# Performance work log

Hardware: AMD Instinct MI355X
Metric: run time of the kernel (lower is better)

## Reference

```python
import jax, jax.numpy as jnp
import numpy as np


def _cell(x, h, c, Wih, Whh, bih, bhh):
    # PyTorch LSTM cell, gate order i, f, g, o
    g = x @ Wih.T + h @ Whh.T + bih + bhh
    i, f, gg, o = jnp.split(g, 4, axis=-1)
    c = jax.nn.sigmoid(f) * c + jax.nn.sigmoid(i) * jnp.tanh(gg)
    h = jax.nn.sigmoid(o) * jnp.tanh(c)
    return h, c


def _run_layer(x, Wih, Whh, bih, bhh):
    # x: (B, T, I) -> (hs (B,T,H), hT (B,H), cT (B,H))
    B = x.shape[0]
    H = Whh.shape[1]
    h0 = jnp.zeros((B, H), x.dtype)
    c0 = jnp.zeros((B, H), x.dtype)

    def step(carry, xt):
        h, c = carry
        h, c = _cell(xt, h, c, Wih, Whh, bih, bhh)
        return (h, c), h

    (hT, cT), hs = jax.lax.scan(step, (h0, c0), jnp.swapaxes(x, 0, 1))
    return jnp.swapaxes(hs, 0, 1), hT, cT


def setup_inputs() -> dict:
    key = jax.random.key(0)
    B, T_HIST, F, H, T_FUT = 16384, 20, 10, 128, 30
    s = 0.08  # ~1/sqrt(hidden) init scale
    ks = jax.random.split(key, 20)
    inp = {
        'hist':   jax.random.normal(ks[0], (B, T_HIST, F), jnp.float32),
        'e_Wih0': jax.random.normal(ks[1], (4 * H, F), jnp.float32) * s,
        'e_Whh0': jax.random.normal(ks[2], (4 * H, H), jnp.float32) * s,
        'e_bih0': jax.random.normal(ks[3], (4 * H,), jnp.float32) * s,
        'e_bhh0': jax.random.normal(ks[4], (4 * H,), jnp.float32) * s,
        'e_Wih1': jax.random.normal(ks[5], (4 * H, H), jnp.float32) * s,
        'e_Whh1': jax.random.normal(ks[6], (4 * H, H), jnp.float32) * s,
        'e_bih1': jax.random.normal(ks[7], (4 * H,), jnp.float32) * s,
        'e_bhh1': jax.random.normal(ks[8], (4 * H,), jnp.float32) * s,
        'd_Wih0': jax.random.normal(ks[9], (4 * H, 2), jnp.float32) * s,
        'd_Whh0': jax.random.normal(ks[10], (4 * H, H), jnp.float32) * s,
        'd_bih0': jax.random.normal(ks[11], (4 * H,), jnp.float32) * s,
        'd_bhh0': jax.random.normal(ks[12], (4 * H,), jnp.float32) * s,
        'd_Wih1': jax.random.normal(ks[13], (4 * H, H), jnp.float32) * s,
        'd_Whh1': jax.random.normal(ks[14], (4 * H, H), jnp.float32) * s,
        'd_bih1': jax.random.normal(ks[15], (4 * H,), jnp.float32) * s,
        'd_bhh1': jax.random.normal(ks[16], (4 * H,), jnp.float32) * s,
        'head_W': jax.random.normal(ks[17], (2, H), jnp.float32) * s,
        'head_b': jax.random.normal(ks[18], (2,), jnp.float32) * s,
        'fut_len': T_FUT,
    }
    return inp


def reference(hist, e_Wih0, e_Whh0, e_bih0, e_bhh0, e_Wih1, e_Whh1, e_bih1, e_bhh1,
              d_Wih0, d_Whh0, d_bih0, d_bhh0, d_Wih1, d_Whh1, d_bih1, d_bhh1,
              head_W, head_b, fut_len):
    B = hist.shape[0]
    # 2-layer encoder over history
    h1, hT0, cT0 = _run_layer(hist, e_Wih0, e_Whh0, e_bih0, e_bhh0)
    _, hT1, cT1 = _run_layer(h1, e_Wih1, e_Whh1, e_bih1, e_bhh1)

    def step(carry, _):
        y, h0, c0, h1_, c1_ = carry
        nh0, nc0 = _cell(y, h0, c0, d_Wih0, d_Whh0, d_bih0, d_bhh0)
        nh1, nc1 = _cell(nh0, h1_, c1_, d_Wih1, d_Whh1, d_bih1, d_bhh1)
        dxy = nh1 @ head_W.T + head_b  # (B, 2)
        return (dxy, nh0, nc0, nh1, nc1), dxy

    y0 = jnp.zeros((B, 2), hist.dtype)
    _, ys = jax.lax.scan(step, (y0, hT0, cT0, hT1, cT1), None, length=fut_len)
    return jnp.swapaxes(ys, 0, 1)  # (B, fut_len, 2)
```

## Files before the change

kernel.cpp:

```cpp
#include <hip/hip_runtime.h>


typedef __attribute__((ext_vector_type(8))) short short8;
typedef __attribute__((ext_vector_type(4))) float float4v;

#define MFMA16(a, b, c) __builtin_amdgcn_mfma_f32_16x16x32_bf16((a), (b), (c), 0, 0, 0)

__device__ __forceinline__ unsigned short f2bf(float x) {
    unsigned u = __builtin_bit_cast(unsigned, x);
    unsigned r = (u + 0x7FFFu + ((u >> 16) & 1u)) >> 16;
    return (unsigned short)r;
}
__device__ __forceinline__ float bf2f(unsigned short b) {
    unsigned u = ((unsigned)b) << 16;
    return __builtin_bit_cast(float, u);
}

#if __has_builtin(__builtin_amdgcn_exp2f)
__device__ __forceinline__ float vexp2(float x) { return __builtin_amdgcn_exp2f(x); }
#else
__device__ __forceinline__ float vexp2(float x) { return exp2f(x); }
#endif
#if __has_builtin(__builtin_amdgcn_rcpf)
__device__ __forceinline__ float vrcp(float x) { return __builtin_amdgcn_rcpf(x); }
#else
__device__ __forceinline__ float vrcp(float x) { return 1.0f / x; }
#endif

__device__ __forceinline__ float sigm(float x) {
    return vrcp(1.0f + vexp2(x * -1.442695040888963f));
}
__device__ __forceinline__ float tanh_(float x) {
    return 1.0f - 2.0f * vrcp(1.0f + vexp2(x * 2.885390081777927f));
}

__global__ void prep_kernel(const float* __restrict__ eWih0, const float* __restrict__ eWhh0,
                            const float* __restrict__ ebih0, const float* __restrict__ ebhh0,
                            const float* __restrict__ eWih1, const float* __restrict__ eWhh1,
                            const float* __restrict__ ebih1, const float* __restrict__ ebhh1,
                            const float* __restrict__ dWih0, const float* __restrict__ dWhh0,
                            const float* __restrict__ dbih0, const float* __restrict__ dbhh0,
                            const float* __restrict__ dWih1, const float* __restrict__ dWhh1,
                            const float* __restrict__ dbih1, const float* __restrict__ dbhh1,
                            void* __restrict__ ws)
{
    int i = blockIdx.x * 256 + threadIdx.x;
    short* We0 = (short*)ws;
    short* We1 = We0 + 512 * 160;
    short* Wd0 = We1 + 512 * 256;
    short* Wd1 = Wd0 + 512 * 128;
    float* bsT = (float*)((char*)ws + 819200);
    float* wyT = bsT + 2048;
    const int N0 = 512 * 160, N1 = 512 * 256, N2 = 512 * 128, N3 = 512 * 256;
    if (i < N0) {
        int n = i / 160, k = i - n * 160;
        float v = (k < 32) ? (k < 10 ? eWih0[n * 10 + k] : 0.0f) : eWhh0[n * 128 + (k - 32)];
        We0[i] = (short)f2bf(v);
    } else if (i < N0 + N1) {
        int ii = i - N0, n = ii >> 8, k = ii & 255;
        float v = (k < 128) ? eWih1[n * 128 + k] : eWhh1[n * 128 + (k - 128)];
        We1[ii] = (short)f2bf(v);
    } else if (i < N0 + N1 + N2) {
        int ii = i - (N0 + N1);
        Wd0[ii] = (short)f2bf(dWhh0[ii]);
    } else if (i < N0 + N1 + N2 + N3) {
        int ii = i - (N0 + N1 + N2), n = ii >> 8, k = ii & 255;
        float v = (k < 128) ? dWih1[n * 128 + k] : dWhh1[n * 128 + (k - 128)];
        Wd1[ii] = (short)f2bf(v);
    } else if (i < N0 + N1 + N2 + N3 + 2048) {
        int ii = i - (N0 + N1 + N2 + N3);
        int set = ii >> 9, r = ii & 511, j = r >> 2, q = r & 3;
        int g = q * 128 + j;
        float v = (set == 0) ? ebih0[g] + ebhh0[g]
                : (set == 1) ? ebih1[g] + ebhh1[g]
                : (set == 2) ? dbih0[g] + dbhh0[g]
                             : dbih1[g] + dbhh1[g];
        bsT[ii] = v;
    } else if (i < N0 + N1 + N2 + N3 + 2048 + 1024) {
        int ii = i - (N0 + N1 + N2 + N3 + 2048);
        int j = ii >> 3, e = ii & 7, q = e >> 1, cc = e & 1;
        wyT[ii] = dWih0[(q * 128 + j) * 2 + cc];
    }
}


template <int NKT>
__device__ __forceinline__ void mma4(float4v acc[4][4], const short8* __restrict__ hb,
                                     const char* __restrict__ wb, const unsigned* wo,
                                     int woff, int nib, int quad)
{
#pragma unroll 1
    for (int kk = 0; kk < NKT; ++kk) {
        int sx = ((kk * 4 + quad) ^ nib) + nib * 16;
        short8 a0 = hb[sx];
        short8 a1 = hb[256 + sx];
        short8 a2 = hb[512 + sx];
        short8 a3 = hb[768 + sx];
        short8 b0 = *(const short8*)(wb + (wo[0] + woff + kk * 64));
        short8 b1 = *(const short8*)(wb + (wo[1] + woff + kk * 64));
        short8 b2 = *(const short8*)(wb + (wo[2] + woff + kk * 64));
        short8 b3 = *(const short8*)(wb + (wo[3] + woff + kk * 64));
        acc[0][0] = MFMA16(a0, b0, acc[0][0]);
        acc[0][1] = MFMA16(a1, b0, acc[0][1]);
        acc[0][2] = MFMA16(a2, b0, acc[0][2]);
        acc[0][3] = MFMA16(a3, b0, acc[0][3]);
        acc[1][0] = MFMA16(a0, b1, acc[1][0]);
        acc[1][1] = MFMA16(a1, b1, acc[1][1]);
        acc[1][2] = MFMA16(a2, b1, acc[1][2]);
        acc[1][3] = MFMA16(a3, b1, acc[1][3]);
        acc[2][0] = MFMA16(a0, b2, acc[2][0]);
        acc[2][1] = MFMA16(a1, b2, acc[2][1]);
        acc[2][2] = MFMA16(a2, b2, acc[2][2]);
        acc[2][3] = MFMA16(a3, b2, acc[2][3]);
        acc[3][0] = MFMA16(a0, b3, acc[3][0]);
        acc[3][1] = MFMA16(a1, b3, acc[3][1]);
        acc[3][2] = MFMA16(a2, b3, acc[3][2]);
        acc[3][3] = MFMA16(a3, b3, acc[3][3]);
    }
}

template <bool DEC0>
__device__ __forceinline__ void cell_update4(float4v acc[4][4], float4v bv,
                                             float* __restrict__ cbase,
                                             unsigned short* __restrict__ hdst,
                                             const float* __restrict__ ybuf,
                                             float4v wy0, float4v wy1,
                                             int j, int quad)
{
    int kc = j >> 3;
    int jl = j & 7;
#pragma unroll
    for (int mt = 0; mt < 4; ++mt) {
#pragma unroll
        for (int r = 0; r < 4; ++r) {
            float gi = acc[0][mt][r] + bv[0];
            float gf = acc[1][mt][r] + bv[1];
            float gg = acc[2][mt][r] + bv[2];
            float go = acc[3][mt][r] + bv[3];
            int m = mt * 16 + quad * 4 + r;
            if (DEC0) {
                float y0 = ybuf[2 * m], y1 = ybuf[2 * m + 1];
                gi += y0 * wy0[0] + y1 * wy0[1];
                gf += y0 * wy0[2] + y1 * wy0[3];
                gg += y0 * wy1[0] + y1 * wy1[1];
                go += y0 * wy1[2] + y1 * wy1[3];
            }
            float si = sigm(gi);
            float sf = sigm(gf);
            float tg = tanh_(gg);
            float so = sigm(go);
            float* cp = cbase + (m * 132 + j);
            float c = sf * (*cp) + si * tg;
            *cp = c;
            float h = so * tanh_(c);
            int slot = m * 16 + (kc ^ (m & 15));
            hdst[slot * 8 + jl] = f2bf(h);
        }
    }
}

__global__ void __attribute__((amdgpu_flat_work_group_size(512, 512), amdgpu_waves_per_eu(2)))
lstm_main(
    const float* __restrict__ hist,
    const float* __restrict__ headW, const float* __restrict__ headB,
    const int* __restrict__ futlen, const void* __restrict__ ws,
    float* __restrict__ out)
{
    __shared__ short8 h0buf[1024];
    __shared__ short8 h1buf[1024];
    __shared__ short8 xbuf[256];
    __shared__ float ybuf[128];
    __shared__ float cbuf0[64 * 132];
    __shared__ float cbuf1[64 * 132];

    const char* wsb = (const char*)ws;
    const char* We0 = wsb;
    const char* We1 = wsb + 512 * 160 * 2;
    const char* Wd0 = We1 + 512 * 256 * 2;
    const char* Wd1 = Wd0 + 512 * 128 * 2;
    const float* bsT = (const float*)(wsb + 819200);
    const float* wyT = bsT + 2048;

    const int tid = threadIdx.x;
    const int w = tid >> 6;
    const int lane = tid & 63;
    const int quad = lane >> 4;
    const int nib = lane & 15;
    const int b0 = blockIdx.x * 64;
    const int TFUT = *futlen;
    const int j = 16 * w + nib;

    h0buf[tid] = (short8)0;
    h0buf[512 + tid] = (short8)0;
    h1buf[tid] = (short8)0;
    h1buf[512 + tid] = (short8)0;
    if (tid < 256) xbuf[tid] = (short8)0;
    if (tid < 128) ybuf[tid] = 0.0f;
    for (int i = tid; i < 64 * 132; i += 512) {
        cbuf0[i] = 0.0f;
        cbuf1[i] = 0.0f;
    }

    unsigned eo0[4], eo1[4];
#pragma unroll
    for (int q = 0; q < 4; ++q) {
        unsigned row = 16u * (w + 8 * q) + nib;
        eo0[q] = row * 320u + quad * 16u;
        eo1[q] = row * 512u + quad * 16u;
    }
    __syncthreads();

#pragma unroll 1
    for (int t = 0; t < 20; ++t) {
        if (tid < 128) {
            int m = tid & 63, part = tid >> 6;
            const float* hp = hist + ((size_t)((b0 + m) * 20 + t)) * 10;
            float v[8];
            if (part == 0) {
#pragma unroll
                for (int i = 0; i < 8; ++i) v[i] = hp[i];
            } else {
                v[0] = hp[8]; v[1] = hp[9];
#pragma unroll
                for (int i = 2; i < 8; ++i) v[i] = 0.0f;
            }
            short8 pk;
#pragma unroll
            for (int i = 0; i < 8; ++i) pk[i] = (short)f2bf(v[i]);
            xbuf[m * 4 + (part ^ (m & 3))] = pk;
        }
        __syncthreads();

        {
            float4v acc[4][4];
#pragma unroll
            for (int q = 0; q < 4; ++q)
#pragma unroll
                for (int mt = 0; mt < 4; ++mt) acc[q][mt] = (float4v){0.f, 0.f, 0.f, 0.f};
            {
                int sxx = (quad ^ (nib & 3)) + nib * 4;
                short8 a0 = xbuf[sxx];
                short8 a1 = xbuf[64 + sxx];
                short8 a2 = xbuf[128 + sxx];
                short8 a3 = xbuf[192 + sxx];
                short8 bq0 = *(const short8*)(We0 + eo0[0]);
                short8 bq1 = *(const short8*)(We0 + eo0[1]);
                short8 bq2 = *(const short8*)(We0 + eo0[2]);
                short8 bq3 = *(const short8*)(We0 + eo0[3]);
                acc[0][0] = MFMA16(a0, bq0, acc[0][0]);
                acc[0][1] = MFMA16(a1, bq0, acc[0][1]);
                acc[0][2] = MFMA16(a2, bq0, acc[0][2]);
                acc[0][3] = MFMA16(a3, bq0, acc[0][3]);
                acc[1][0] = MFMA16(a0, bq1, acc[1][0]);
                acc[1][1] = MFMA16(a1, bq1, acc[1][1]);
                acc[1][2] = MFMA16(a2, bq1, acc[1][2]);
                acc[1][3] = MFMA16(a3, bq1, acc[1][3]);
                acc[2][0] = MFMA16(a0, bq2, acc[2][0]);
                acc[2][1] = MFMA16(a1, bq2, acc[2][1]);
                acc[2][2] = MFMA16(a2, bq2, acc[2][2]);
                acc[2][3] = MFMA16(a3, bq2, acc[2][3]);
                acc[3][0] = MFMA16(a0, bq3, acc[3][0]);
                acc[3][1] = MFMA16(a1, bq3, acc[3][1]);
                acc[3][2] = MFMA16(a2, bq3, acc[3][2]);
                acc[3][3] = MFMA16(a3, bq3, acc[3][3]);
            }
            mma4<4>(acc, h0buf, We0, eo0, 64, nib, quad);
            float4v bv = *(const float4v*)(bsT + 0 * 512 + j * 4);
            __syncthreads();
            cell_update4<false>(acc, bv, cbuf0, (unsigned short*)h0buf, nullptr,
                                (float4v){0, 0, 0, 0}, (float4v){0, 0, 0, 0}, j, quad);
        }
        __syncthreads();

        {
            float4v acc[4][4];
#pragma unroll
            for (int q = 0; q < 4; ++q)
#pragma unroll
                for (int mt = 0; mt < 4; ++mt) acc[q][mt] = (float4v){0.f, 0.f, 0.f, 0.f};
            mma4<4>(acc, h0buf, We1, eo1, 0, nib, quad);
            mma4<4>(acc, h1buf, We1, eo1, 256, nib, quad);
            float4v bv = *(const float4v*)(bsT + 1 * 512 + j * 4);
            __syncthreads();
            cell_update4<false>(acc, bv, cbuf1, (unsigned short*)h1buf, nullptr,
                                (float4v){0, 0, 0, 0}, (float4v){0, 0, 0, 0}, j, quad);
        }
        __syncthreads();
    }

    unsigned do0[4];
#pragma unroll
    for (int q = 0; q < 4; ++q) {
        unsigned row = 16u * (w + 8 * q) + nib;
        do0[q] = row * 256u + quad * 16u;
    }

#pragma unroll 1
    for (int t = 0; t < TFUT; ++t) {
        {
            float4v acc[4][4];
#pragma unroll
            for (int q = 0; q < 4; ++q)
#pragma unroll
                for (int mt = 0; mt < 4; ++mt) acc[q][mt] = (float4v){0.f, 0.f, 0.f, 0.f};
            mma4<4>(acc, h0buf, Wd0, do0, 0, nib, quad);
            float4v bv = *(const float4v*)(bsT + 2 * 512 + j * 4);
            float4v wy0 = *(const float4v*)(wyT + j * 8);
            float4v wy1 = *(const float4v*)(wyT + j * 8 + 4);
            __syncthreads();
            cell_update4<true>(acc, bv, cbuf0, (unsigned short*)h0buf, ybuf, wy0, wy1, j, quad);
        }
        __syncthreads();

        {
            float4v acc[4][4];
#pragma unroll
            for (int q = 0; q < 4; ++q)
#pragma unroll
                for (int mt = 0; mt < 4; ++mt) acc[q][mt] = (float4v){0.f, 0.f, 0.f, 0.f};
            mma4<4>(acc, h0buf, Wd1, eo1, 0, nib, quad);
            mma4<4>(acc, h1buf, Wd1, eo1, 256, nib, quad);
            float4v bv = *(const float4v*)(bsT + 3 * 512 + j * 4);
            __syncthreads();
            cell_update4<false>(acc, bv, cbuf1, (unsigned short*)h1buf, nullptr,
                                (float4v){0, 0, 0, 0}, (float4v){0, 0, 0, 0}, j, quad);
        }
        __syncthreads();

        if (tid < 128) {
            int m = tid & 63, jj = tid >> 6;
            const float4v* hw = (const float4v*)(headW + jj * 128);
            float dot = headB[jj];
            int mk = m & 15;
#pragma unroll
            for (int kc = 0; kc < 16; ++kc) {
                short8 ch = h1buf[m * 16 + (kc ^ mk)];
                float4v w0 = hw[kc * 2], w1 = hw[kc * 2 + 1];
                dot += bf2f((unsigned short)ch[0]) * w0[0];
                dot += bf2f((unsigned short)ch[1]) * w0[1];
                dot += bf2f((unsigned short)ch[2]) * w0[2];
                dot += bf2f((unsigned short)ch[3]) * w0[3];
                dot += bf2f((unsigned short)ch[4]) * w1[0];
                dot += bf2f((unsigned short)ch[5]) * w1[1];
                dot += bf2f((unsigned short)ch[6]) * w1[2];
                dot += bf2f((unsigned short)ch[7]) * w1[3];
            }
            ybuf[2 * m + jj] = dot;
            out[((size_t)(b0 + m) * TFUT + t) * 2 + jj] = dot;
        }
        __syncthreads();
    }
}

extern "C" void kernel_launch(void* const* d_in, const int* in_sizes, int n_in,
                              void* d_out, int out_size, void* d_ws, size_t ws_size,
                              hipStream_t stream)
{
    const float* hist   = (const float*)d_in[0];
    const float* eWih0  = (const float*)d_in[1];
    const float* eWhh0  = (const float*)d_in[2];
    const float* ebih0  = (const float*)d_in[3];
    const float* ebhh0  = (const float*)d_in[4];
    const float* eWih1  = (const float*)d_in[5];
    const float* eWhh1  = (const float*)d_in[6];
    const float* ebih1  = (const float*)d_in[7];
    const float* ebhh1  = (const float*)d_in[8];
    const float* dWih0  = (const float*)d_in[9];
    const float* dWhh0  = (const float*)d_in[10];
    const float* dbih0  = (const float*)d_in[11];
    const float* dbhh0  = (const float*)d_in[12];
    const float* dWih1  = (const float*)d_in[13];
    const float* dWhh1  = (const float*)d_in[14];
    const float* dbih1  = (const float*)d_in[15];
    const float* dbhh1  = (const float*)d_in[16];
    const float* headW  = (const float*)d_in[17];
    const float* headB  = (const float*)d_in[18];
    const int*   futlen = (const int*)d_in[19];

    prep_kernel<<<1612, 256, 0, stream>>>(eWih0, eWhh0, ebih0, ebhh0,
                                          eWih1, eWhh1, ebih1, ebhh1,
                                          dWih0, dWhh0, dbih0, dbhh0,
                                          dWih1, dWhh1, dbih1, dbhh1, d_ws);

    lstm_main<<<256, 512, 0, stream>>>(hist, headW, headB, futlen,
                                       d_ws, (float*)d_out);
}
```

Measured before the change: 946.7 us.

## Double-buffer LSTM hidden states and prefetch weights to remove intra-step barriers

Hidden-state and input LDS buffers become ping-pong pairs, so each cell update writes the alternate buffer and the barrier between the MMA reads and the state writes is removed. The next timestep's history input is loaded and packed after the layer-0 barrier instead of with its own barrier. The weight-fragment loop in mma4 is fully unrolled, and the next k-slice of weights is software-prefetched while the current MFMAs run. This doubles the h/x shared-memory footprint, which may limit blocks per CU and raises register pressure.

```diff
diff --git a/kernel.cpp b/kernel.cpp
--- a/kernel.cpp
+++ b/kernel.cpp
@@ -89,17 +89,24 @@
                                      const char* __restrict__ wb, const unsigned* wo,
                                      int woff, int nib, int quad)
 {
-#pragma unroll 1
+    const char* pb = wb + woff;
+    short8 b0 = *(const short8*)(pb + wo[0]);
+    short8 b1 = *(const short8*)(pb + wo[1]);
+    short8 b2 = *(const short8*)(pb + wo[2]);
+    short8 b3 = *(const short8*)(pb + wo[3]);
+#pragma unroll
     for (int kk = 0; kk < NKT; ++kk) {
         int sx = ((kk * 4 + quad) ^ nib) + nib * 16;
         short8 a0 = hb[sx];
         short8 a1 = hb[256 + sx];
         short8 a2 = hb[512 + sx];
         short8 a3 = hb[768 + sx];
-        short8 b0 = *(const short8*)(wb + (wo[0] + woff + kk * 64));
-        short8 b1 = *(const short8*)(wb + (wo[1] + woff + kk * 64));
-        short8 b2 = *(const short8*)(wb + (wo[2] + woff + kk * 64));
-        short8 b3 = *(const short8*)(wb + (wo[3] + woff + kk * 64));
+        short8 n0 = b0, n1 = b1, n2 = b2, n3 = b3;
+        if (kk + 1 < NKT) {
+            const char* pn = wb + woff + (kk + 1) * 64;
+            n0 = *(const short8*)(pn + wo[0]);
+            n1 = *(const short8*)(pn + wo[1]);
+        }
         acc[0][0] = MFMA16(a0, b0, acc[0][0]);
         acc[0][1] = MFMA16(a1, b0, acc[0][1]);
         acc[0][2] = MFMA16(a2, b0, acc[0][2]);
@@ -108,6 +115,11 @@
         acc[1][1] = MFMA16(a1, b1, acc[1][1]);
         acc[1][2] = MFMA16(a2, b1, acc[1][2]);
         acc[1][3] = MFMA16(a3, b1, acc[1][3]);
+        if (kk + 1 < NKT) {
+            const char* pn = wb + woff + (kk + 1) * 64;
+            n2 = *(const short8*)(pn + wo[2]);
+            n3 = *(const short8*)(pn + wo[3]);
+        }
         acc[2][0] = MFMA16(a0, b2, acc[2][0]);
         acc[2][1] = MFMA16(a1, b2, acc[2][1]);
         acc[2][2] = MFMA16(a2, b2, acc[2][2]);
@@ -116,6 +128,7 @@
         acc[3][1] = MFMA16(a1, b3, acc[3][1]);
         acc[3][2] = MFMA16(a2, b3, acc[3][2]);
         acc[3][3] = MFMA16(a3, b3, acc[3][3]);
+        b0 = n0; b1 = n1; b2 = n2; b3 = n3;
     }
 }
 
@@ -166,9 +179,9 @@
     const int* __restrict__ futlen, const void* __restrict__ ws,
     float* __restrict__ out)
 {
-    __shared__ short8 h0buf[1024];
-    __shared__ short8 h1buf[1024];
-    __shared__ short8 xbuf[256];
+    __shared__ short8 h0buf[2][1024];
+    __shared__ short8 h1buf[2][1024];
+    __shared__ short8 xbuf[2][256];
     __shared__ float ybuf[128];
     __shared__ float cbuf0[64 * 132];
     __shared__ float cbuf1[64 * 132];
@@ -190,16 +203,35 @@
     const int TFUT = *futlen;
     const int j = 16 * w + nib;
 
-    h0buf[tid] = (short8)0;
-    h0buf[512 + tid] = (short8)0;
-    h1buf[tid] = (short8)0;
-    h1buf[512 + tid] = (short8)0;
-    if (tid < 256) xbuf[tid] = (short8)0;
+    h0buf[0][tid] = (short8)0;
+    h0buf[0][512 + tid] = (short8)0;
+    h1buf[0][tid] = (short8)0;
+    h1buf[0][512 + tid] = (short8)0;
+    ((short8*)xbuf)[tid] = (short8)0;
     if (tid < 128) ybuf[tid] = 0.0f;
     for (int i = tid; i < 64 * 132; i += 512) {
         cbuf0[i] = 0.0f;
         cbuf1[i] = 0.0f;
     }
+    __syncthreads();
+
+    if (tid < 128) {
+        int m = tid & 63, part = tid >> 6;
+        const float* hp = hist + ((size_t)((b0 + m) * 20 + 0)) * 10;
+        float v[8];
+        if (part == 0) {
+#pragma unroll
+            for (int i = 0; i < 8; ++i) v[i] = hp[i];
+        } else {
+            v[0] = hp[8]; v[1] = hp[9];
+#pragma unroll
+            for (int i = 2; i < 8; ++i) v[i] = 0.0f;
+        }
+        short8 pk;
+#pragma unroll
+        for (int i = 0; i < 8; ++i) pk[i] = (short)f2bf(v[i]);
+        xbuf[0][m * 4 + (part ^ (m & 3))] = pk;
+    }
 
     unsigned eo0[4], eo1[4];
 #pragma unroll
@@ -208,29 +240,11 @@
         eo0[q] = row * 320u + quad * 16u;
         eo1[q] = row * 512u + quad * 16u;
     }
+    int p0 = 0, p1 = 0, px = 0;
     __syncthreads();
 
 #pragma unroll 1
     for (int t = 0; t < 20; ++t) {
-        if (tid < 128) {
-            int m = tid & 63, part = tid >> 6;
-            const float* hp = hist + ((size_t)((b0 + m) * 20 + t)) * 10;
-            float v[8];
-            if (part == 0) {
-#pragma unroll
-                for (int i = 0; i < 8; ++i) v[i] = hp[i];
-            } else {
-                v[0] = hp[8]; v[1] = hp[9];
-#pragma unroll
-                for (int i = 2; i < 8; ++i) v[i] = 0.0f;
-            }
-            short8 pk;
-#pragma unroll
-            for (int i = 0; i < 8; ++i) pk[i] = (short)f2bf(v[i]);
-            xbuf[m * 4 + (part ^ (m & 3))] = pk;
-        }
-        __syncthreads();
-
         {
             float4v acc[4][4];
 #pragma unroll
@@ -238,11 +252,12 @@
 #pragma unroll
                 for (int mt = 0; mt < 4; ++mt) acc[q][mt] = (float4v){0.f, 0.f, 0.f, 0.f};
             {
+                const short8* xb = xbuf[px];
                 int sxx = (quad ^ (nib & 3)) + nib * 4;
-                short8 a0 = xbuf[sxx];
-                short8 a1 = xbuf[64 + sxx];
-                short8 a2 = xbuf[128 + sxx];
-                short8 a3 = xbuf[192 + sxx];
+                short8 a0 = xb[sxx];
+                short8 a1 = xb[64 + sxx];
+                short8 a2 = xb[128 + sxx];
+                short8 a3 = xb[192 + sxx];
                 short8 bq0 = *(const short8*)(We0 + eo0[0]);
                 short8 bq1 = *(const short8*)(We0 + eo0[1]);
                 short8 bq2 = *(const short8*)(We0 + eo0[2]);
@@ -264,13 +279,30 @@
                 acc[3][2] = MFMA16(a2, bq3, acc[3][2]);
                 acc[3][3] = MFMA16(a3, bq3, acc[3][3]);
             }
-            mma4<4>(acc, h0buf, We0, eo0, 64, nib, quad);
+            mma4<4>(acc, h0buf[p0], We0, eo0, 64, nib, quad);
             float4v bv = *(const float4v*)(bsT + 0 * 512 + j * 4);
-            __syncthreads();
-            cell_update4<false>(acc, bv, cbuf0, (unsigned short*)h0buf, nullptr,
+            cell_update4<false>(acc, bv, cbuf0, (unsigned short*)h0buf[p0 ^ 1], nullptr,
                                 (float4v){0, 0, 0, 0}, (float4v){0, 0, 0, 0}, j, quad);
         }
         __syncthreads();
+
+        if (tid < 128 && t < 19) {
+            int m = tid & 63, part = tid >> 6;
+            const float* hp = hist + ((size_t)((b0 + m) * 20 + (t + 1))) * 10;
+            float v[8];
+            if (part == 0) {
+#pragma unroll
+                for (int i = 0; i < 8; ++i) v[i] = hp[i];
+            } else {
+                v[0] = hp[8]; v[1] = hp[9];
+#pragma unroll
+                for (int i = 2; i < 8; ++i) v[i] = 0.0f;
+            }
+            short8 pk;
+#pragma unroll
+            for (int i = 0; i < 8; ++i) pk[i] = (short)f2bf(v[i]);
+            xbuf[px ^ 1][m * 4 + (part ^ (m & 3))] = pk;
+        }
 
         {
             float4v acc[4][4];
@@ -278,14 +310,14 @@
             for (int q = 0; q < 4; ++q)
 #pragma unroll
                 for (int mt = 0; mt < 4; ++mt) acc[q][mt] = (float4v){0.f, 0.f, 0.f, 0.f};
-            mma4<4>(acc, h0buf, We1, eo1, 0, nib, quad);
-            mma4<4>(acc, h1buf, We1, eo1, 256, nib, quad);
+            mma4<4>(acc, h0buf[p0 ^ 1], We1, eo1, 0, nib, quad);
+            mma4<4>(acc, h1buf[p1], We1, eo1, 256, nib, quad);
             float4v bv = *(const float4v*)(bsT + 1 * 512 + j * 4);
-            __syncthreads();
-            cell_update4<false>(acc, bv, cbuf1, (unsigned short*)h1buf, nullptr,
+            cell_update4<false>(acc, bv, cbuf1, (unsigned short*)h1buf[p1 ^ 1], nullptr,
                                 (float4v){0, 0, 0, 0}, (float4v){0, 0, 0, 0}, j, quad);
         }
         __syncthreads();
+        p0 ^= 1; p1 ^= 1; px ^= 1;
     }
 
     unsigned do0[4];
@@ -303,12 +335,12 @@
             for (int q = 0; q < 4; ++q)
 #pragma unroll
                 for (int mt = 0; mt < 4; ++mt) acc[q][mt] = (float4v){0.f, 0.f, 0.f, 0.f};
-            mma4<4>(acc, h0buf, Wd0, do0, 0, nib, quad);
+            mma4<4>(acc, h0buf[p0], Wd0, do0, 0, nib, quad);
             float4v bv = *(const float4v*)(bsT + 2 * 512 + j * 4);
             float4v wy0 = *(const float4v*)(wyT + j * 8);
             float4v wy1 = *(const float4v*)(wyT + j * 8 + 4);
-            __syncthreads();
-            cell_update4<true>(acc, bv, cbuf0, (unsigned short*)h0buf, ybuf, wy0, wy1, j, quad);
+            cell_update4<true>(acc, bv, cbuf0, (unsigned short*)h0buf[p0 ^ 1],
+                               ybuf, wy0, wy1, j, quad);
         }
         __syncthreads();
 
@@ -318,23 +350,23 @@
             for (int q = 0; q < 4; ++q)
 #pragma unroll
                 for (int mt = 0; mt < 4; ++mt) acc[q][mt] = (float4v){0.f, 0.f, 0.f, 0.f};
-            mma4<4>(acc, h0buf, Wd1, eo1, 0, nib, quad);
-            mma4<4>(acc, h1buf, Wd1, eo1, 256, nib, quad);
+            mma4<4>(acc, h0buf[p0 ^ 1], Wd1, eo1, 0, nib, quad);
+            mma4<4>(acc, h1buf[p1], Wd1, eo1, 256, nib, quad);
             float4v bv = *(const float4v*)(bsT + 3 * 512 + j * 4);
-            __syncthreads();
-            cell_update4<false>(acc, bv, cbuf1, (unsigned short*)h1buf, nullptr,
+            cell_update4<false>(acc, bv, cbuf1, (unsigned short*)h1buf[p1 ^ 1], nullptr,
                                 (float4v){0, 0, 0, 0}, (float4v){0, 0, 0, 0}, j, quad);
         }
         __syncthreads();
 
         if (tid < 128) {
             int m = tid & 63, jj = tid >> 6;
+            const short8* hb = h1buf[p1 ^ 1];
             const float4v* hw = (const float4v*)(headW + jj * 128);
             float dot = headB[jj];
             int mk = m & 15;
 #pragma unroll
             for (int kc = 0; kc < 16; ++kc) {
-                short8 ch = h1buf[m * 16 + (kc ^ mk)];
+                short8 ch = hb[m * 16 + (kc ^ mk)];
                 float4v w0 = hw[kc * 2], w1 = hw[kc * 2 + 1];
                 dot += bf2f((unsigned short)ch[0]) * w0[0];
                 dot += bf2f((unsigned short)ch[1]) * w0[1];
@@ -349,6 +381,7 @@
             out[((size_t)(b0 + m) * TFUT + t) * 2 + jj] = dot;
         }
         __syncthreads();
+        p0 ^= 1; p1 ^= 1;
     }
 }
 
```

Result: slower. 1.105 ms (+16.8%).
